# Performance work log

Hardware: AMD Instinct MI355X
Metric: run time of the kernel (lower is better)

## Reference

```python
import jax, jax.numpy as jnp
import numpy as np

SEG = 512        # segment_size
DIL = 2          # dilation_rate
LN_EPS = 1e-5


def _layer_norm(x, gamma, beta):
    mu = jnp.mean(x, axis=-1, keepdims=True)
    var = jnp.var(x, axis=-1, keepdims=True)
    return (x - mu) * jax.lax.rsqrt(var + LN_EPS) * gamma + beta


def setup_inputs() -> dict:
    key = jax.random.key(0)
    ks = jax.random.split(key, 5)
    B, N, D = 4, 4096, 1024
    s = 0.02
    return {
        "x": jax.random.normal(ks[0], (B, N, D), dtype=jnp.float32),
        "Wq": jax.random.normal(ks[1], (D, D), dtype=jnp.float32) * s,
        "Wk": jax.random.normal(ks[2], (D, D), dtype=jnp.float32) * s,
        "Wv": jax.random.normal(ks[3], (D, D), dtype=jnp.float32) * s,
        "Wo": jax.random.normal(ks[4], (D, D), dtype=jnp.float32) * s,
        "gamma": jnp.ones((D,), dtype=jnp.float32),
        "beta": jnp.zeros((D,), dtype=jnp.float32),
    }


def reference(x, Wq, Wk, Wv, Wo, gamma, beta):
    B, N, D = x.shape
    n_seg = N // SEG
    s = SEG // DIL  # tokens per segment after dilation
    # strided dilated gather: [B, n_seg, s, D]
    xs = x.reshape(B, n_seg, SEG, D)[:, :, ::DIL, :]
    # torch Linear(bias=False): x @ W.T ; then LayerNorm on each of q,k,v
    q = _layer_norm(jnp.einsum('bgsd,ed->bgse', xs, Wq), gamma, beta)
    k = _layer_norm(jnp.einsum('bgsd,ed->bgse', xs, Wk), gamma, beta)
    v = _layer_norm(jnp.einsum('bgsd,ed->bgse', xs, Wv), gamma, beta)
    # causal SDPA with head_dim = D (no head split in the original code)
    scale = 1.0 / jnp.sqrt(jnp.asarray(D, dtype=q.dtype))
    scores = jnp.einsum('bgqd,bgkd->bgqk', q, k) * scale  # [B, n_seg, s, s]
    causal = jnp.tril(jnp.ones((s, s), dtype=bool))
    scores = jnp.where(causal, scores, jnp.finfo(scores.dtype).min)
    attn = jax.nn.softmax(scores, axis=-1)
    y = jnp.einsum('bgqk,bgkd->bgqd', attn, v)  # [B, n_seg, s, D]
    y = y.reshape(B, N // DIL, D)
    # strided scatter into zero-initialized full tensor
    y_full = jnp.zeros((B, N, D), dtype=y.dtype).at[:, ::DIL, :].set(y)
    out = jnp.einsum('bnd,ed->bne', y_full, Wo)
    return out
```

## Files before the change

kernel.cpp:

```cpp
#include <hip/hip_runtime.h>
#include <stdint.h>

typedef __bf16 bf16_t;
typedef __bf16 bf16x8 __attribute__((ext_vector_type(8)));
typedef __bf16 bf16x4 __attribute__((ext_vector_type(4)));
typedef float  f32x4  __attribute__((ext_vector_type(4)));


__device__ __forceinline__ void gload16(const void* g, void* lds)
{
    __builtin_amdgcn_global_load_lds(
        (__attribute__((address_space(1))) void*)(void*)g,
        (__attribute__((address_space(3))) void*)lds,
        16, 0, 0);
}

__device__ __forceinline__ f32x4 mfma16(bf16x8 a, bf16x8 b, f32x4 c)
{
    return __builtin_amdgcn_mfma_f32_16x16x32_bf16(a, b, c, 0, 0, 0);
}

#define SBAR()   asm volatile("s_barrier" ::: "memory")
#define LGKM0()  asm volatile("s_waitcnt lgkmcnt(0)" ::: "memory")
#define VMCNT(N) asm volatile("s_waitcnt vmcnt(" #N ")" ::: "memory")


__global__ __launch_bounds__(256)
void cast_weights(const float* __restrict__ Wq, const float* __restrict__ Wk,
                  const float* __restrict__ Wv, const float* __restrict__ Wo,
                  bf16_t* __restrict__ Wqkv, bf16_t* __restrict__ Wob)
{
    const int which = blockIdx.x >> 10;
    const int blk   = blockIdx.x & 1023;
    const float* src = which == 0 ? Wq : which == 1 ? Wk : which == 2 ? Wv : Wo;
    bf16_t* dst = which == 3 ? Wob : Wqkv + (size_t)which * 1048576;
    const size_t i = ((size_t)blk * 256 + threadIdx.x) * 4;
    float4 f = *(const float4*)&src[i];
    bf16x4 o;
    o[0] = (bf16_t)f.x; o[1] = (bf16_t)f.y; o[2] = (bf16_t)f.z; o[3] = (bf16_t)f.w;
    *(bf16x4*)&dst[i] = o;
}

__global__ __launch_bounds__(256)
void gather_cast_x(const float* __restrict__ x, bf16_t* __restrict__ Xe)
{
    const int m = blockIdx.x;
    const int b = m >> 11, g = (m >> 8) & 7, j = m & 255;
    const float* src = x + ((size_t)b * 4096 + g * 512 + 2 * j) * 1024;
    bf16_t* dst = Xe + (size_t)m * 1024;
    const int t = threadIdx.x;
    float4 f = *(const float4*)&src[t * 4];
    bf16x4 o;
    o[0] = (bf16_t)f.x; o[1] = (bf16_t)f.y; o[2] = (bf16_t)f.z; o[3] = (bf16_t)f.w;
    *(bf16x4*)&dst[t * 4] = o;
}

template<int EPI>
__global__ __launch_bounds__(512, 2)
void gemm256x128(const bf16_t* __restrict__ A, const bf16_t* __restrict__ B,
                 void* __restrict__ Cv, int K, int lda, int ldb, int ldc)
{
    __shared__ __align__(16) char lds[98304];

    const int tid = threadIdx.x;
    const int w = tid >> 6, lane = tid & 63;
    const int wr = w >> 2, wc = w & 3;
    const int fr = lane & 15, fg = lane >> 4;
    const int bn = blockIdx.x, bm = blockIdx.y;
    const int NT = K >> 6;

    const int s = tid ^ ((tid >> 3) & 7);
    const char* srcA = (const char*)A + ((size_t)(bm * 256 + (s >> 3)) * lda + (s & 7) * 8) * 2;
    const char* srcB = (const char*)B + ((size_t)(bn * 128 + (s >> 3)) * ldb + (s & 7) * 8) * 2;
    const size_t aStep = (size_t)64 * lda * 2;
    const size_t bStep = (size_t)64 * ldb * 2;
    const int ldsW = w * 1024;

#define STG_A(T, Q) gload16(srcA + (Q) * aStep + (size_t)(T) * 128, \
                            lds + ((T) & 1) * 49152 + (Q) * 8192 + ldsW)
#define STG_B(T, U) gload16(srcB + (U) * bStep + (size_t)(T) * 128, \
                            lds + ((T) & 1) * 49152 + 32768 + (U) * 8192 + ldsW)

    const int flip = (fr & 7) << 4;
    const int aoff = (wr * 128 + fr) * 128 + fg * 16;
    const int boff = 32768 + (wc * 32 + fr) * 128 + fg * 16;

    bf16x8 a[4][2], b[2][2];
    f32x4 acc[8][2] = {};

#define LDA(PH, CB) do {                                                        \
    _Pragma("unroll") for (int mi = 0; mi < 4; ++mi)                            \
    _Pragma("unroll") for (int ks = 0; ks < 2; ++ks)                            \
        a[mi][ks] = *(const bf16x8*)(lds + (CB) +                               \
            ((aoff + (PH) * 8192 + mi * 2048 + ks * 64) ^ flip));               \
} while (0)

#define LDB(CB) do {                                                            \
    _Pragma("unroll") for (int ni = 0; ni < 2; ++ni)                            \
    _Pragma("unroll") for (int ks = 0; ks < 2; ++ks)                            \
        b[ni][ks] = *(const bf16x8*)(lds + (CB) +                               \
            ((boff + ni * 2048 + ks * 64) ^ flip));                             \
} while (0)

#define MF(PH) do {                                                             \
    _Pragma("unroll") for (int mi = 0; mi < 4; ++mi)                            \
    _Pragma("unroll") for (int ni = 0; ni < 2; ++ni)                            \
    _Pragma("unroll") for (int ks = 0; ks < 2; ++ks)                            \
        acc[(PH) * 4 + mi][ni] =                                                \
            mfma16(b[ni][ks], a[mi][ks], acc[(PH) * 4 + mi][ni]);               \
} while (0)

    STG_A(0, 0); STG_A(0, 1); STG_A(0, 2); STG_A(0, 3); STG_B(0, 0); STG_B(0, 1);
    STG_A(1, 0); STG_A(1, 2); STG_B(1, 0); STG_B(1, 1);
    VMCNT(4);
    SBAR();

    for (int t = 0; t < NT - 2; ++t) {
        const int cb = (t & 1) * 49152;
        LDA(0, cb); LDB(cb);
        STG_A(t + 1, 1); STG_A(t + 1, 3);
        SBAR(); LGKM0();
        __builtin_amdgcn_s_setprio(1); MF(0); __builtin_amdgcn_s_setprio(0);
        VMCNT(6);
        SBAR();
        LDA(1, cb);
        STG_A(t + 2, 0); STG_A(t + 2, 2); STG_B(t + 2, 0); STG_B(t + 2, 1);
        SBAR(); LGKM0();
        __builtin_amdgcn_s_setprio(1); MF(1); __builtin_amdgcn_s_setprio(0);
        VMCNT(6);
        SBAR();
    }

    {
        const int cb = ((NT - 2) & 1) * 49152;
        LDA(0, cb); LDB(cb);
        STG_A(NT - 1, 1); STG_A(NT - 1, 3);
        SBAR(); LGKM0();
        MF(0);
        VMCNT(6);
        SBAR();
        LDA(1, cb);
        SBAR(); LGKM0();
        MF(1);
        VMCNT(0);
        SBAR();
    }
    {
        const int cb = ((NT - 1) & 1) * 49152;
        LDA(0, cb); LDB(cb);
        LGKM0();
        MF(0);
        LDA(1, cb);
        LGKM0();
        MF(1);
    }

#undef STG_A
#undef STG_B
#undef LDA
#undef LDB
#undef MF

    const int r0 = bm * 256 + wr * 128 + fr;
    const int c0 = bn * 128 + wc * 32 + fg * 4;
    if constexpr (EPI == 0) {
        bf16_t* C = (bf16_t*)Cv;
#pragma unroll
        for (int mig = 0; mig < 8; ++mig)
#pragma unroll
            for (int ni = 0; ni < 2; ++ni) {
                const int row = r0 + (mig >> 2) * 64 + (mig & 3) * 16;
                bf16x4 o;
#pragma unroll
                for (int r = 0; r < 4; ++r) o[r] = (bf16_t)acc[mig][ni][r];
                *(bf16x4*)&C[(size_t)row * ldc + c0 + ni * 16] = o;
            }
    } else {
        float* C = (float*)Cv;
        const f32x4 z4 = {0.f, 0.f, 0.f, 0.f};
#pragma unroll
        for (int mig = 0; mig < 8; ++mig)
#pragma unroll
            for (int ni = 0; ni < 2; ++ni) {
                const int m  = r0 + (mig >> 2) * 64 + (mig & 3) * 16;
                const int gr = ((m >> 11) << 12) | (((m >> 8) & 7) << 9) | ((m & 255) << 1);
                *(f32x4*)&C[(size_t)gr * 1024 + c0 + ni * 16]       = acc[mig][ni];
                *(f32x4*)&C[(size_t)(gr + 1) * 1024 + c0 + ni * 16] = z4;
            }
    }
}

template<int EPI>
__global__ __launch_bounds__(256)
void gemm_nt(const bf16_t* __restrict__ A, const bf16_t* __restrict__ B,
             void* __restrict__ Cv,
             int K, int lda, int ldb, int ldc,
             long sA, long sB, long sC, int flags)
{
    __shared__ __align__(16) bf16_t Asm[128 * 32];
    __shared__ __align__(16) bf16_t Bsm[128 * 32];

    const int bn = blockIdx.x, bm = blockIdx.y, bz = blockIdx.z;
    if ((flags & 2) && bn > bm) return;

    const int tid  = threadIdx.x;
    const int wave = tid >> 6;
    const int lane = tid & 63;
    const int wr = wave >> 1, wc = wave & 1;

    const bf16_t* Ab = A + (long)bz * sA;
    const bf16_t* Bb = B + (long)bz * sB;

    const int Keff = ((flags & 1) && bm == 0) ? (K >> 1) : K;

    const int sw0 = tid ^ ((tid >> 3) & 3);
    const int dd1 = tid + 256;
    const int sw1 = dd1 ^ ((dd1 >> 3) & 3);
    const bf16_t* a0 = Ab + (size_t)(bm * 128 + (sw0 >> 2)) * lda + (sw0 & 3) * 8;
    const bf16_t* a1 = Ab + (size_t)(bm * 128 + (sw1 >> 2)) * lda + (sw1 & 3) * 8;
    const bf16_t* b0 = Bb + (size_t)(bn * 128 + (sw0 >> 2)) * ldb + (sw0 & 3) * 8;
    const bf16_t* b1 = Bb + (size_t)(bn * 128 + (sw1 >> 2)) * ldb + (sw1 & 3) * 8;
    char* ldsA = (char*)Asm + wave * 1024;
    char* ldsB = (char*)Bsm + wave * 1024;

    f32x4 acc[4][4] = {};

    const int frow = lane & 15;
    const int fk   = (lane >> 4) * 8;
    const int flip = (frow & 6) << 2;

    for (int k0 = 0; k0 < Keff; k0 += 32) {
        gload16(a0, ldsA);
        gload16(a1, ldsA + 4096);
        gload16(b0, ldsB);
        gload16(b1, ldsB + 4096);
        a0 += 32; a1 += 32; b0 += 32; b1 += 32;
        __syncthreads();

        bf16x8 af[4], bfr[4];
#pragma unroll
        for (int mi = 0; mi < 4; ++mi)
            af[mi] = *(const bf16x8*)&Asm[(size_t)(((wr * 64 + mi * 16 + frow) * 32 + fk) ^ flip)];
#pragma unroll
        for (int ni = 0; ni < 4; ++ni)
            bfr[ni] = *(const bf16x8*)&Bsm[(size_t)(((wc * 64 + ni * 16 + frow) * 32 + fk) ^ flip)];
#pragma unroll
        for (int mi = 0; mi < 4; ++mi)
#pragma unroll
            for (int ni = 0; ni < 4; ++ni)
                acc[mi][ni] = mfma16(bfr[ni], af[mi], acc[mi][ni]);
        __syncthreads();
    }

    const int row0 = bm * 128 + wr * 64 + frow;
    const int col0 = bn * 128 + wc * 64 + (lane >> 4) * 4;

    if constexpr (EPI == 0) {
        bf16_t* C = (bf16_t*)Cv + (long)bz * sC;
#pragma unroll
        for (int mi = 0; mi < 4; ++mi)
#pragma unroll
            for (int ni = 0; ni < 4; ++ni) {
                bf16x4 o;
#pragma unroll
                for (int r = 0; r < 4; ++r) o[r] = (bf16_t)acc[mi][ni][r];
                *(bf16x4*)&C[(size_t)(row0 + mi * 16) * ldc + col0 + ni * 16] = o;
            }
    } else {
        float* C = (float*)Cv + (long)bz * sC;
#pragma unroll
        for (int mi = 0; mi < 4; ++mi)
#pragma unroll
            for (int ni = 0; ni < 4; ++ni)
                *(f32x4*)&C[(size_t)(row0 + mi * 16) * ldc + col0 + ni * 16] = acc[mi][ni];
    }
}

__global__ __launch_bounds__(256)
void ln_kernel(bf16_t* __restrict__ qkv,
               const float* __restrict__ gamma, const float* __restrict__ beta)
{
    const int row = blockIdx.x;
    const int which = blockIdx.y;
    bf16_t* p = qkv + (size_t)row * 3072 + which * 1024;
    const int t = threadIdx.x;

    bf16x4 v = *(const bf16x4*)&p[t * 4];
    float f[4];
    float s = 0.f, ss = 0.f;
#pragma unroll
    for (int i = 0; i < 4; ++i) { f[i] = (float)v[i]; s += f[i]; ss += f[i] * f[i]; }
#pragma unroll
    for (int o = 32; o; o >>= 1) { s += __shfl_xor(s, o); ss += __shfl_xor(ss, o); }

    __shared__ float rs_[4], rss_[4];
    const int wave = t >> 6, lane = t & 63;
    if (lane == 0) { rs_[wave] = s; rss_[wave] = ss; }
    __syncthreads();
    s  = rs_[0] + rs_[1] + rs_[2] + rs_[3];
    ss = rss_[0] + rss_[1] + rss_[2] + rss_[3];

    const float mu   = s * (1.f / 1024.f);
    const float var  = ss * (1.f / 1024.f) - mu * mu;
    const float rstd = rsqrtf(var + 1e-5f);

    bf16x4 o;
#pragma unroll
    for (int i = 0; i < 4; ++i) {
        const int c = t * 4 + i;
        o[i] = (bf16_t)((f[i] - mu) * rstd * gamma[c] + beta[c]);
    }
    *(bf16x4*)&p[t * 4] = o;
}

__global__ __launch_bounds__(256)
void softmax_kernel(const float* __restrict__ S, bf16_t* __restrict__ P)
{
    const int q = blockIdx.x & 255;
    const size_t base = (size_t)blockIdx.x * 256;
    const int c = threadIdx.x;
    const bool ok = (c <= q);

    float v = ok ? S[base + c] * (1.f / 32.f) : -3.0e38f;
    float m = v;
#pragma unroll
    for (int o = 32; o; o >>= 1) m = fmaxf(m, __shfl_xor(m, o));

    __shared__ float rm[4], rsum[4];
    const int wave = c >> 6, lane = c & 63;
    if (lane == 0) rm[wave] = m;
    __syncthreads();
    m = fmaxf(fmaxf(rm[0], rm[1]), fmaxf(rm[2], rm[3]));

    float e = ok ? __expf(v - m) : 0.f;
    float s = e;
#pragma unroll
    for (int o = 32; o; o >>= 1) s += __shfl_xor(s, o);
    if (lane == 0) rsum[wave] = s;
    __syncthreads();
    s = rsum[0] + rsum[1] + rsum[2] + rsum[3];

    P[base + c] = (bf16_t)(e / s);
}

__global__ __launch_bounds__(256)
void transpose_v(const bf16_t* __restrict__ Vn, bf16_t* __restrict__ Vt)
{
    __shared__ bf16_t tile[32][33];
    const int seg = blockIdx.z;
    const int e0 = blockIdx.x * 32, k0 = blockIdx.y * 32;
    const int xx = threadIdx.x, yy = threadIdx.y;
    const bf16_t* src = Vn + (size_t)seg * 256 * 3072;
#pragma unroll
    for (int i = 0; i < 32; i += 8)
        tile[yy + i][xx] = src[(size_t)(k0 + yy + i) * 3072 + e0 + xx];
    __syncthreads();
    bf16_t* dst = Vt + (size_t)seg * 262144;
#pragma unroll
    for (int i = 0; i < 32; i += 8)
        dst[(size_t)(e0 + yy + i) * 256 + k0 + xx] = tile[xx][yy + i];
}


extern "C" void kernel_launch(void* const* d_in, const int* in_sizes, int n_in,
                              void* d_out, int out_size, void* d_ws, size_t ws_size,
                              hipStream_t stream)
{
    const float* x     = (const float*)d_in[0];
    const float* Wq    = (const float*)d_in[1];
    const float* Wk    = (const float*)d_in[2];
    const float* Wv    = (const float*)d_in[3];
    const float* Wo    = (const float*)d_in[4];
    const float* gamma = (const float*)d_in[5];
    const float* beta  = (const float*)d_in[6];
    float* out = (float*)d_out;

    char* ws = (char*)d_ws;
    bf16_t* Xe   = (bf16_t*)(ws);
    bf16_t* Wqkv = (bf16_t*)(ws + (16u  << 20));
    bf16_t* Wob  = (bf16_t*)(ws + (22u  << 20));
    bf16_t* QKV  = (bf16_t*)(ws + (24u  << 20));
    float*  Smat = (float*) (ws + (72u  << 20));
    bf16_t* P    = (bf16_t*)(ws + (80u  << 20));
    bf16_t* Vt   = (bf16_t*)(ws + (84u  << 20));
    bf16_t* Y    = (bf16_t*)(ws + (100u << 20));

    cast_weights<<<4096, 256, 0, stream>>>(Wq, Wk, Wv, Wo, Wqkv, Wob);
    gather_cast_x<<<8192, 256, 0, stream>>>(x, Xe);

    gemm256x128<0><<<dim3(24, 32), 512, 0, stream>>>(
        Xe, Wqkv, QKV, 1024, 1024, 1024, 3072);

    ln_kernel<<<dim3(8192, 3), 256, 0, stream>>>(QKV, gamma, beta);

    gemm_nt<1><<<dim3(2, 2, 32), 256, 0, stream>>>(
        QKV, QKV + 1024, Smat, 1024, 3072, 3072, 256,
        256L * 3072, 256L * 3072, 65536L, 2);

    softmax_kernel<<<8192, 256, 0, stream>>>(Smat, P);

    transpose_v<<<dim3(32, 8, 32), dim3(32, 8), 0, stream>>>(QKV + 2048, Vt);

    gemm_nt<0><<<dim3(8, 2, 32), 256, 0, stream>>>(
        P, Vt, Y, 256, 256, 256, 1024,
        65536L, 262144L, 262144L, 1);

    gemm256x128<2><<<dim3(8, 32), 512, 0, stream>>>(
        Y, Wob, out, 1024, 1024, 1024, 1024);
}
```

Before: 201.9 us.

## Merge prep kernels, multi-tile QKV GEMM, fuse QK^T with V transpose

Several independent changes. The two cast kernels become one launch. The QKV GEMM becomes a persistent multi-subtile kernel in which each block loops over three N tiles, with a grid remap meant to improve L2 locality and fewer blocks overall. The QK^T GEMM and the V transpose share one launch through a new kernel that computes only the causal lower-triangle tiles. LayerNorm handles two rows per block with 8-wide vectors. Together these cut launch count and raise per-block work, at the cost of 256 blocks for the QKV GEMM, which may underfill the GPU, and more complex epilogue scheduling inside the main loop.

Result: faster. 173.8 us (-13.9%).

```diff
diff --git a/kernel.cpp b/kernel.cpp
--- a/kernel.cpp
+++ b/kernel.cpp
@@ -26,39 +26,40 @@
 
 
 __global__ __launch_bounds__(256)
-void cast_weights(const float* __restrict__ Wq, const float* __restrict__ Wk,
-                  const float* __restrict__ Wv, const float* __restrict__ Wo,
-                  bf16_t* __restrict__ Wqkv, bf16_t* __restrict__ Wob)
-{
-    const int which = blockIdx.x >> 10;
-    const int blk   = blockIdx.x & 1023;
-    const float* src = which == 0 ? Wq : which == 1 ? Wk : which == 2 ? Wv : Wo;
-    bf16_t* dst = which == 3 ? Wob : Wqkv + (size_t)which * 1048576;
-    const size_t i = ((size_t)blk * 256 + threadIdx.x) * 4;
-    float4 f = *(const float4*)&src[i];
-    bf16x4 o;
-    o[0] = (bf16_t)f.x; o[1] = (bf16_t)f.y; o[2] = (bf16_t)f.z; o[3] = (bf16_t)f.w;
-    *(bf16x4*)&dst[i] = o;
-}
-
-__global__ __launch_bounds__(256)
-void gather_cast_x(const float* __restrict__ x, bf16_t* __restrict__ Xe)
-{
-    const int m = blockIdx.x;
-    const int b = m >> 11, g = (m >> 8) & 7, j = m & 255;
-    const float* src = x + ((size_t)b * 4096 + g * 512 + 2 * j) * 1024;
-    bf16_t* dst = Xe + (size_t)m * 1024;
+void prep_kernel(const float* __restrict__ Wq, const float* __restrict__ Wk,
+                 const float* __restrict__ Wv, const float* __restrict__ Wo,
+                 const float* __restrict__ x,
+                 bf16_t* __restrict__ Wqkv, bf16_t* __restrict__ Wob,
+                 bf16_t* __restrict__ Xe)
+{
+    const int bid = blockIdx.x;
     const int t = threadIdx.x;
-    float4 f = *(const float4*)&src[t * 4];
-    bf16x4 o;
-    o[0] = (bf16_t)f.x; o[1] = (bf16_t)f.y; o[2] = (bf16_t)f.z; o[3] = (bf16_t)f.w;
-    *(bf16x4*)&dst[t * 4] = o;
-}
-
-template<int EPI>
+    if (bid < 4096) {
+        const int which = bid >> 10;
+        const int blk = bid & 1023;
+        const float* src = which == 0 ? Wq : which == 1 ? Wk : which == 2 ? Wv : Wo;
+        bf16_t* dst = which == 3 ? Wob : Wqkv + (size_t)which * 1048576;
+        const size_t i = ((size_t)blk * 256 + t) * 4;
+        float4 f = *(const float4*)&src[i];
+        bf16x4 o;
+        o[0] = (bf16_t)f.x; o[1] = (bf16_t)f.y; o[2] = (bf16_t)f.z; o[3] = (bf16_t)f.w;
+        *(bf16x4*)&dst[i] = o;
+    } else {
+        const int m = bid - 4096;
+        const int b = m >> 11, g = (m >> 8) & 7, j = m & 255;
+        const float* src = x + ((size_t)b * 4096 + g * 512 + 2 * j) * 1024;
+        bf16_t* dst = Xe + (size_t)m * 1024;
+        float4 f = *(const float4*)&src[t * 4];
+        bf16x4 o;
+        o[0] = (bf16_t)f.x; o[1] = (bf16_t)f.y; o[2] = (bf16_t)f.z; o[3] = (bf16_t)f.w;
+        *(bf16x4*)&dst[t * 4] = o;
+    }
+}
+
+template<int EPI, int NSUB>
 __global__ __launch_bounds__(512, 2)
-void gemm256x128(const bf16_t* __restrict__ A, const bf16_t* __restrict__ B,
-                 void* __restrict__ Cv, int K, int lda, int ldb, int ldc)
+void gemm_mt(const bf16_t* __restrict__ A, const bf16_t* __restrict__ B,
+             void* __restrict__ Cv, int lda, int ldb, int ldc)
 {
     __shared__ __align__(16) char lds[98304];
 
@@ -66,19 +67,24 @@
     const int w = tid >> 6, lane = tid & 63;
     const int wr = w >> 2, wc = w & 3;
     const int fr = lane & 15, fg = lane >> 4;
-    const int bn = blockIdx.x, bm = blockIdx.y;
-    const int NT = K >> 6;
+
+    const int lin = blockIdx.y * 8 + blockIdx.x;
+    const int L = (lin & 7) * 32 + (lin >> 3);
+    const int bm = L >> 3, j = L & 7;
+    const int NT = NSUB * 16;
 
     const int s = tid ^ ((tid >> 3) & 7);
-    const char* srcA = (const char*)A + ((size_t)(bm * 256 + (s >> 3)) * lda + (s & 7) * 8) * 2;
-    const char* srcB = (const char*)B + ((size_t)(bn * 128 + (s >> 3)) * ldb + (s & 7) * 8) * 2;
-    const size_t aStep = (size_t)64 * lda * 2;
-    const size_t bStep = (size_t)64 * ldb * 2;
+    const char* srcA  = (const char*)A + ((size_t)(bm * 256 + (s >> 3)) * lda + (s & 7) * 8) * 2;
+    const char* srcB0 = (const char*)B + ((size_t)(j * NSUB * 128 + (s >> 3)) * ldb + (s & 7) * 8) * 2;
+    const size_t aStep  = (size_t)64 * lda * 2;
+    const size_t bStep  = (size_t)64 * ldb * 2;
+    const size_t bnStep = (size_t)128 * ldb * 2;
     const int ldsW = w * 1024;
 
-#define STG_A(T, Q) gload16(srcA + (Q) * aStep + (size_t)(T) * 128, \
+#define STG_A(T, Q) gload16(srcA + (Q) * aStep + (size_t)((T) & 15) * 128,          \
                             lds + ((T) & 1) * 49152 + (Q) * 8192 + ldsW)
-#define STG_B(T, U) gload16(srcB + (U) * bStep + (size_t)(T) * 128, \
+#define STG_B(T, U) gload16(srcB0 + (size_t)((T) >> 4) * bnStep + (U) * bStep       \
+                                  + (size_t)((T) & 15) * 128,                        \
                             lds + ((T) & 1) * 49152 + 32768 + (U) * 8192 + ldsW)
 
     const int flip = (fr & 7) << 4;
@@ -108,6 +114,36 @@
     _Pragma("unroll") for (int ks = 0; ks < 2; ++ks)                            \
         acc[(PH) * 4 + mi][ni] =                                                \
             mfma16(b[ni][ks], a[mi][ks], acc[(PH) * 4 + mi][ni]);               \
+} while (0)
+
+    const int r0 = bm * 256 + wr * 128 + fr;
+    const int c0w = wc * 32 + fg * 4;
+
+#define DO_EPI(SUB) do {                                                                  \
+    const int _c0 = (j * NSUB + (SUB)) * 128 + c0w;                                       \
+    if constexpr (EPI == 0) {                                                             \
+        bf16_t* C = (bf16_t*)Cv;                                                          \
+        _Pragma("unroll") for (int mig = 0; mig < 8; ++mig)                               \
+        _Pragma("unroll") for (int ni = 0; ni < 2; ++ni) {                                \
+            const int row = r0 + (mig >> 2) * 64 + (mig & 3) * 16;                        \
+            bf16x4 o;                                                                     \
+            _Pragma("unroll") for (int r = 0; r < 4; ++r) o[r] = (bf16_t)acc[mig][ni][r]; \
+            *(bf16x4*)&C[(size_t)row * ldc + _c0 + ni * 16] = o;                          \
+        }                                                                                 \
+    } else {                                                                              \
+        float* C = (float*)Cv;                                                            \
+        const f32x4 z4 = {0.f, 0.f, 0.f, 0.f};                                            \
+        _Pragma("unroll") for (int mig = 0; mig < 8; ++mig)                               \
+        _Pragma("unroll") for (int ni = 0; ni < 2; ++ni) {                                \
+            const int m  = r0 + (mig >> 2) * 64 + (mig & 3) * 16;                         \
+            const int gr = ((m >> 11) << 12) | (((m >> 8) & 7) << 9) | ((m & 255) << 1);  \
+            *(f32x4*)&C[(size_t)gr * 1024 + _c0 + ni * 16]       = acc[mig][ni];          \
+            *(f32x4*)&C[(size_t)(gr + 1) * 1024 + _c0 + ni * 16] = z4;                    \
+        }                                                                                 \
+    }                                                                                     \
+    _Pragma("unroll") for (int mig = 0; mig < 8; ++mig)                                   \
+    _Pragma("unroll") for (int ni = 0; ni < 2; ++ni)                                      \
+        acc[mig][ni] = (f32x4){0.f, 0.f, 0.f, 0.f};                                       \
 } while (0)
 
     STG_A(0, 0); STG_A(0, 1); STG_A(0, 2); STG_A(0, 3); STG_B(0, 0); STG_B(0, 1);
@@ -128,6 +164,7 @@
         SBAR(); LGKM0();
         __builtin_amdgcn_s_setprio(1); MF(1); __builtin_amdgcn_s_setprio(0);
         VMCNT(6);
+        if ((t & 15) == 15) DO_EPI(t >> 4);
         SBAR();
     }
 
@@ -154,40 +191,14 @@
         LGKM0();
         MF(1);
     }
+    DO_EPI(NSUB - 1);
 
 #undef STG_A
 #undef STG_B
 #undef LDA
 #undef LDB
 #undef MF
-
-    const int r0 = bm * 256 + wr * 128 + fr;
-    const int c0 = bn * 128 + wc * 32 + fg * 4;
-    if constexpr (EPI == 0) {
-        bf16_t* C = (bf16_t*)Cv;
-#pragma unroll
-        for (int mig = 0; mig < 8; ++mig)
-#pragma unroll
-            for (int ni = 0; ni < 2; ++ni) {
-                const int row = r0 + (mig >> 2) * 64 + (mig & 3) * 16;
-                bf16x4 o;
-#pragma unroll
-                for (int r = 0; r < 4; ++r) o[r] = (bf16_t)acc[mig][ni][r];
-                *(bf16x4*)&C[(size_t)row * ldc + c0 + ni * 16] = o;
-            }
-    } else {
-        float* C = (float*)Cv;
-        const f32x4 z4 = {0.f, 0.f, 0.f, 0.f};
-#pragma unroll
-        for (int mig = 0; mig < 8; ++mig)
-#pragma unroll
-            for (int ni = 0; ni < 2; ++ni) {
-                const int m  = r0 + (mig >> 2) * 64 + (mig & 3) * 16;
-                const int gr = ((m >> 11) << 12) | (((m >> 8) & 7) << 9) | ((m & 255) << 1);
-                *(f32x4*)&C[(size_t)gr * 1024 + c0 + ni * 16]       = acc[mig][ni];
-                *(f32x4*)&C[(size_t)(gr + 1) * 1024 + c0 + ni * 16] = z4;
-            }
-    }
+#undef DO_EPI
 }
 
 template<int EPI>
@@ -201,8 +212,6 @@
     __shared__ __align__(16) bf16_t Bsm[128 * 32];
 
     const int bn = blockIdx.x, bm = blockIdx.y, bz = blockIdx.z;
-    if ((flags & 2) && bn > bm) return;
-
     const int tid  = threadIdx.x;
     const int wave = tid >> 6;
     const int lane = tid & 63;
@@ -277,19 +286,116 @@
 }
 
 __global__ __launch_bounds__(256)
+void qk_tr_kernel(const bf16_t* __restrict__ qkv, float* __restrict__ Smat,
+                  bf16_t* __restrict__ Vt)
+{
+    __shared__ __align__(16) char smem[16384];
+    const int bid = blockIdx.x;
+    const int tid = threadIdx.x;
+
+    if (bid < 96) {
+        const int seg = bid / 3, r = bid % 3;
+        const int bm = (r + 1) >> 1, bn = r >> 1;
+        const bf16_t* Ab = qkv + (size_t)seg * 256 * 3072;
+        const bf16_t* Bb = Ab + 1024;
+        bf16_t* Asm = (bf16_t*)smem;
+        bf16_t* Bsm = Asm + 4096;
+
+        const int wave = tid >> 6, lane = tid & 63;
+        const int wr = wave >> 1, wc = wave & 1;
+        const int sw0 = tid ^ ((tid >> 3) & 3);
+        const int dd1 = tid + 256;
+        const int sw1 = dd1 ^ ((dd1 >> 3) & 3);
+        const bf16_t* a0 = Ab + (size_t)(bm * 128 + (sw0 >> 2)) * 3072 + (sw0 & 3) * 8;
+        const bf16_t* a1 = Ab + (size_t)(bm * 128 + (sw1 >> 2)) * 3072 + (sw1 & 3) * 8;
+        const bf16_t* b0 = Bb + (size_t)(bn * 128 + (sw0 >> 2)) * 3072 + (sw0 & 3) * 8;
+        const bf16_t* b1 = Bb + (size_t)(bn * 128 + (sw1 >> 2)) * 3072 + (sw1 & 3) * 8;
+        char* ldsA = (char*)Asm + wave * 1024;
+        char* ldsB = (char*)Bsm + wave * 1024;
+
+        f32x4 acc[4][4] = {};
+        const int frow = lane & 15;
+        const int fk   = (lane >> 4) * 8;
+        const int flip = (frow & 6) << 2;
+
+        for (int k0 = 0; k0 < 1024; k0 += 32) {
+            gload16(a0, ldsA);
+            gload16(a1, ldsA + 4096);
+            gload16(b0, ldsB);
+            gload16(b1, ldsB + 4096);
+            a0 += 32; a1 += 32; b0 += 32; b1 += 32;
+            __syncthreads();
+
+            bf16x8 af[4], bfr[4];
+#pragma unroll
+            for (int mi = 0; mi < 4; ++mi)
+                af[mi] = *(const bf16x8*)&Asm[(size_t)(((wr * 64 + mi * 16 + frow) * 32 + fk) ^ flip)];
+#pragma unroll
+            for (int ni = 0; ni < 4; ++ni)
+                bfr[ni] = *(const bf16x8*)&Bsm[(size_t)(((wc * 64 + ni * 16 + frow) * 32 + fk) ^ flip)];
+#pragma unroll
+            for (int mi = 0; mi < 4; ++mi)
+#pragma unroll
+                for (int ni = 0; ni < 4; ++ni)
+                    acc[mi][ni] = mfma16(bfr[ni], af[mi], acc[mi][ni]);
+            __syncthreads();
+        }
+
+        float* C = Smat + (size_t)seg * 65536;
+        const int row0 = bm * 128 + wr * 64 + frow;
+        const int col0 = bn * 128 + wc * 64 + (lane >> 4) * 4;
+#pragma unroll
+        for (int mi = 0; mi < 4; ++mi)
+#pragma unroll
+            for (int ni = 0; ni < 4; ++ni)
+                *(f32x4*)&C[(size_t)(row0 + mi * 16) * 256 + col0 + ni * 16] = acc[mi][ni];
+    } else {
+        const int id2 = bid - 96;
+        const int seg = id2 >> 6;
+        const int rem = id2 & 63;
+        const int eb = rem >> 2, kb = rem & 3;
+        bf16_t* tile = (bf16_t*)smem;
+
+        const int rr = tid >> 2, cs = (tid & 3) * 16;
+        const bf16_t* src = qkv + ((size_t)(seg * 256 + kb * 64 + rr)) * 3072
+                                + 2048 + eb * 64 + cs;
+        bf16x8 v0 = *(const bf16x8*)&src[0];
+        bf16x8 v1 = *(const bf16x8*)&src[8];
+#pragma unroll
+        for (int i = 0; i < 8; ++i) {
+            tile[rr * 65 + cs + i]     = v0[i];
+            tile[rr * 65 + cs + 8 + i] = v1[i];
+        }
+        __syncthreads();
+        bf16x8 o0, o1;
+#pragma unroll
+        for (int i = 0; i < 8; ++i) {
+            o0[i] = tile[(cs + i) * 65 + rr];
+            o1[i] = tile[(cs + 8 + i) * 65 + rr];
+        }
+        bf16_t* dst = Vt + (size_t)seg * 262144 + (size_t)(eb * 64 + rr) * 256 + kb * 64 + cs;
+        *(bf16x8*)&dst[0] = o0;
+        *(bf16x8*)&dst[8] = o1;
+    }
+}
+
+__global__ __launch_bounds__(256)
 void ln_kernel(bf16_t* __restrict__ qkv,
                const float* __restrict__ gamma, const float* __restrict__ beta)
 {
-    const int row = blockIdx.x;
+    const int t = threadIdx.x;
+    const int r = t >> 7;
+    const int row = blockIdx.x * 2 + r;
     const int which = blockIdx.y;
     bf16_t* p = qkv + (size_t)row * 3072 + which * 1024;
-    const int t = threadIdx.x;
-
-    bf16x4 v = *(const bf16x4*)&p[t * 4];
-    float f[4];
+    const int li = t & 127;
+    const int c0 = li * 8;
+
+    bf16x8 v = *(const bf16x8*)&p[c0];
+    float f[8];
     float s = 0.f, ss = 0.f;
 #pragma unroll
-    for (int i = 0; i < 4; ++i) { f[i] = (float)v[i]; s += f[i]; ss += f[i] * f[i]; }
+    for (int i = 0; i < 8; ++i) { f[i] = (float)v[i]; s += f[i]; ss += f[i] * f[i]; }
 #pragma unroll
     for (int o = 32; o; o >>= 1) { s += __shfl_xor(s, o); ss += __shfl_xor(ss, o); }
 
@@ -297,20 +403,18 @@
     const int wave = t >> 6, lane = t & 63;
     if (lane == 0) { rs_[wave] = s; rss_[wave] = ss; }
     __syncthreads();
-    s  = rs_[0] + rs_[1] + rs_[2] + rs_[3];
-    ss = rss_[0] + rss_[1] + rss_[2] + rss_[3];
+    s  = rs_[2 * r] + rs_[2 * r + 1];
+    ss = rss_[2 * r] + rss_[2 * r + 1];
 
     const float mu   = s * (1.f / 1024.f);
     const float var  = ss * (1.f / 1024.f) - mu * mu;
     const float rstd = rsqrtf(var + 1e-5f);
 
-    bf16x4 o;
-#pragma unroll
-    for (int i = 0; i < 4; ++i) {
-        const int c = t * 4 + i;
-        o[i] = (bf16_t)((f[i] - mu) * rstd * gamma[c] + beta[c]);
-    }
-    *(bf16x4*)&p[t * 4] = o;
+    bf16x8 o;
+#pragma unroll
+    for (int i = 0; i < 8; ++i)
+        o[i] = (bf16_t)((f[i] - mu) * rstd * gamma[c0 + i] + beta[c0 + i]);
+    *(bf16x8*)&p[c0] = o;
 }
 
 __global__ __launch_bounds__(256)
@@ -341,24 +445,6 @@
     s = rsum[0] + rsum[1] + rsum[2] + rsum[3];
 
     P[base + c] = (bf16_t)(e / s);
-}
-
-__global__ __launch_bounds__(256)
-void transpose_v(const bf16_t* __restrict__ Vn, bf16_t* __restrict__ Vt)
-{
-    __shared__ bf16_t tile[32][33];
-    const int seg = blockIdx.z;
-    const int e0 = blockIdx.x * 32, k0 = blockIdx.y * 32;
-    const int xx = threadIdx.x, yy = threadIdx.y;
-    const bf16_t* src = Vn + (size_t)seg * 256 * 3072;
-#pragma unroll
-    for (int i = 0; i < 32; i += 8)
-        tile[yy + i][xx] = src[(size_t)(k0 + yy + i) * 3072 + e0 + xx];
-    __syncthreads();
-    bf16_t* dst = Vt + (size_t)seg * 262144;
-#pragma unroll
-    for (int i = 0; i < 32; i += 8)
-        dst[(size_t)(e0 + yy + i) * 256 + k0 + xx] = tile[xx][yy + i];
 }
 
 
@@ -385,26 +471,21 @@
     bf16_t* Vt   = (bf16_t*)(ws + (84u  << 20));
     bf16_t* Y    = (bf16_t*)(ws + (100u << 20));
 
-    cast_weights<<<4096, 256, 0, stream>>>(Wq, Wk, Wv, Wo, Wqkv, Wob);
-    gather_cast_x<<<8192, 256, 0, stream>>>(x, Xe);
-
-    gemm256x128<0><<<dim3(24, 32), 512, 0, stream>>>(
-        Xe, Wqkv, QKV, 1024, 1024, 1024, 3072);
-
-    ln_kernel<<<dim3(8192, 3), 256, 0, stream>>>(QKV, gamma, beta);
-
-    gemm_nt<1><<<dim3(2, 2, 32), 256, 0, stream>>>(
-        QKV, QKV + 1024, Smat, 1024, 3072, 3072, 256,
-        256L * 3072, 256L * 3072, 65536L, 2);
+    prep_kernel<<<12288, 256, 0, stream>>>(Wq, Wk, Wv, Wo, x, Wqkv, Wob, Xe);
+
+    gemm_mt<0, 3><<<dim3(8, 32), 512, 0, stream>>>(
+        Xe, Wqkv, QKV, 1024, 1024, 3072);
+
+    ln_kernel<<<dim3(4096, 3), 256, 0, stream>>>(QKV, gamma, beta);
+
+    qk_tr_kernel<<<96 + 2048, 256, 0, stream>>>(QKV, Smat, Vt);
 
     softmax_kernel<<<8192, 256, 0, stream>>>(Smat, P);
-
-    transpose_v<<<dim3(32, 8, 32), dim3(32, 8), 0, stream>>>(QKV + 2048, Vt);
 
     gemm_nt<0><<<dim3(8, 2, 32), 256, 0, stream>>>(
         P, Vt, Y, 256, 256, 256, 1024,
         65536L, 262144L, 262144L, 1);
 
-    gemm256x128<2><<<dim3(8, 32), 512, 0, stream>>>(
-        Y, Wob, out, 1024, 1024, 1024, 1024);
-}
+    gemm_mt<2, 1><<<dim3(8, 32), 512, 0, stream>>>(
+        Y, Wob, out, 1024, 1024, 1024);
+}
```
